# Kernel tuning notes

Hardware: AMD Instinct MI355X
Metric: run time of the kernel (lower is better)

Reference implementation:

```python
import jax, jax.numpy as jnp
import numpy as np

B, T, C = 4, 2048, 1024
N_HEAD = 16
HEAD_SIZE = C // N_HEAD


def setup_inputs() -> dict:
    key = jax.random.key(0)
    ks = jax.random.split(key, 9)
    std = 0.02
    return {
        "x": jax.random.normal(ks[0], (B, T, C), dtype=jnp.float32),
        "Wk": jax.random.normal(ks[1], (C, C), dtype=jnp.float32) * std,
        "bk": jnp.zeros((C,), dtype=jnp.float32),
        "Wq": jax.random.normal(ks[2], (C, C), dtype=jnp.float32) * std,
        "bq": jnp.zeros((C,), dtype=jnp.float32),
        "Wv": jax.random.normal(ks[3], (C, C), dtype=jnp.float32) * std,
        "bv": jnp.zeros((C,), dtype=jnp.float32),
        "Wo": jax.random.normal(ks[4], (C, C), dtype=jnp.float32) * std,
        "bo": jnp.zeros((C,), dtype=jnp.float32),
    }


def reference(x, Wk, bk, Wq, bq, Wv, bv, Wo, bo):
    # QKV projections -> (B, T, H, D)
    k = (x @ Wk + bk).reshape(B, T, N_HEAD, HEAD_SIZE)
    q = (x @ Wq + bq).reshape(B, T, N_HEAD, HEAD_SIZE)
    v = (x @ Wv + bv).reshape(B, T, N_HEAD, HEAD_SIZE)
    # Scaled causal attention scores: (B, H, T, T)
    scale = 1.0 / jnp.sqrt(jnp.asarray(HEAD_SIZE, dtype=x.dtype))
    scores = jnp.einsum("bqhd,bkhd->bhqk", q, k) * scale
    causal = jnp.tril(jnp.ones((T, T), dtype=bool))
    scores = jnp.where(causal, scores, jnp.asarray(-1e10, dtype=x.dtype))
    probs = jax.nn.softmax(scores, axis=-1)
    # Weighted values -> (B, T, H, D) -> (B, T, C)
    y = jnp.einsum("bhqk,bkhd->bqhd", probs, v).reshape(B, T, C)
    # Output projection (dropout rates are 0 / deterministic)
    return y @ Wo + bo
```

## Files before the change

kernel.cpp:

```cpp
#include <hip/hip_runtime.h>
#include <hip/hip_bf16.h>

typedef unsigned short ushort_t;
typedef __attribute__((ext_vector_type(8))) short short8;
typedef __attribute__((ext_vector_type(4))) float floatx4;

#define BATCH 4
#define SEQ   2048
#define CH    1024
#define NHEAD 16
#define HSZ   64
#define MROWS (BATCH * SEQ)

#define GLD16(gptr, lptr) \
    __builtin_amdgcn_global_load_lds((const __attribute__((address_space(1))) unsigned int*)(gptr), \
                                     (__attribute__((address_space(3))) unsigned int*)(lptr), 16, 0, 0)

__device__ inline ushort_t f2b(float f) {
    __hip_bfloat16 h = __float2bfloat16(f);
    return *(ushort_t*)&h;
}
__device__ inline float b2f(ushort_t u) {
    return __bfloat162float(*(__hip_bfloat16*)&u);
}

__global__ void detect_dtype(const ushort_t* __restrict__ x, int* __restrict__ flag) {
    if (threadIdx.x == 0 && blockIdx.x == 0) {
        int cnt = 0;
        for (int i = 0; i < 512; i++) {
            const int e = (x[2 * i] >> 7) & 0xFF;
            if (e >= 100 && e <= 140) cnt++;
        }
        *flag = (cnt >= 400) ? 1 : 0;
    }
}

__global__ __launch_bounds__(256) void convert_wt4(const void* w0, const void* w1,
                                                   const void* w2, const void* w3,
                                                   ushort_t* o0, ushort_t* o1,
                                                   ushort_t* o2, ushort_t* o3,
                                                   const int* __restrict__ flag) {
    __shared__ ushort_t tile[32][33];
    const void* in = (blockIdx.z == 0) ? w0 : (blockIdx.z == 1) ? w1 : (blockIdx.z == 2) ? w2 : w3;
    ushort_t*  out = (blockIdx.z == 0) ? o0 : (blockIdx.z == 1) ? o1 : (blockIdx.z == 2) ? o2 : o3;
    const int am = *flag;
    const int bx = blockIdx.x * 32, by = blockIdx.y * 32;
    const int tx = threadIdx.x & 31, ty = threadIdx.x >> 5;
    #pragma unroll
    for (int r = ty; r < 32; r += 8) {
        const size_t idx = (size_t)(by + r) * CH + bx + tx;
        tile[r][tx] = am ? ((const ushort_t*)in)[idx] : f2b(((const float*)in)[idx]);
    }
    __syncthreads();
    #pragma unroll
    for (int r = ty; r < 32; r += 8)
        out[(size_t)(bx + r) * CH + by + tx] = tile[tx][r];
}

__global__ void convert_bias4(const void* b0, const void* b1, const void* b2, const void* b3,
                              ushort_t* __restrict__ out, const int* __restrict__ flag) {
    const int i = blockIdx.x * 256 + threadIdx.x;
    const int m = i >> 10, idx = i & 1023;
    const void* in = (m == 0) ? b0 : (m == 1) ? b1 : (m == 2) ? b2 : b3;
    out[i] = (*flag) ? ((const ushort_t*)in)[idx] : f2b(((const float*)in)[idx]);
}

__global__ __launch_bounds__(256) void convert_x(const void* __restrict__ in,
                                                 ushort_t* __restrict__ out,
                                                 const int* __restrict__ flag) {
    const int i = (blockIdx.x * 256 + threadIdx.x) * 8;
    if (*flag) {
        *(float4*)&out[i] = *(const float4*)&((const ushort_t*)in)[i];
    } else {
        const float* p = (const float*)in + i;
        float4 f0 = *(const float4*)p;
        float4 f1 = *(const float4*)(p + 4);
        ushort_t t[8] = {f2b(f0.x), f2b(f0.y), f2b(f0.z), f2b(f0.w),
                         f2b(f1.x), f2b(f1.y), f2b(f1.z), f2b(f1.w)};
        *(float4*)&out[i] = *(const float4*)t;
    }
}

__global__ __launch_bounds__(256) void gemm_qkv(const ushort_t* __restrict__ A,
                                                const ushort_t* __restrict__ Bt,
                                                const ushort_t* __restrict__ bias,
                                                ushort_t* __restrict__ Qb,
                                                ushort_t* __restrict__ Kb,
                                                ushort_t* __restrict__ Vt,
                                                float qscale) {
    __shared__ __align__(16) ushort_t As[128 * 32];
    __shared__ __align__(16) ushort_t Bs[128 * 32];
    const int K = CH;
    const int tid = threadIdx.x;
    const int lane = tid & 63, wave = tid >> 6;
    const int lane15 = lane & 15, quad = lane >> 4;
    const int wr = (wave >> 1) * 64, wc = (wave & 1) * 64;
    const int row0 = blockIdx.x * 128, col0 = blockIdx.y * 128;
    const int seg = blockIdx.y >> 3;

    floatx4 acc[4][4];
    #pragma unroll
    for (int i = 0; i < 4; i++)
        #pragma unroll
        for (int j = 0; j < 4; j++) acc[i][j] = {0.f, 0.f, 0.f, 0.f};

    for (int k0 = 0; k0 < K; k0 += 32) {
        #pragma unroll
        for (int l = wave; l < 8; l += 4) {
            GLD16(A  + (size_t)(row0 + l * 16 + (lane >> 2)) * K + k0 + (lane & 3) * 8, &As[l * 512]);
            GLD16(Bt + (size_t)(col0 + l * 16 + (lane >> 2)) * K + k0 + (lane & 3) * 8, &Bs[l * 512]);
        }
        __syncthreads();
        short8 af[4], bfr[4];
        #pragma unroll
        for (int i = 0; i < 4; i++)
            af[i] = *(const short8*)&As[(wr + i * 16 + lane15) * 32 + quad * 8];
        #pragma unroll
        for (int j = 0; j < 4; j++)
            bfr[j] = *(const short8*)&Bs[(wc + j * 16 + lane15) * 32 + quad * 8];
        #pragma unroll
        for (int i = 0; i < 4; i++)
            #pragma unroll
            for (int j = 0; j < 4; j++)
                acc[i][j] = __builtin_amdgcn_mfma_f32_16x16x32_bf16(af[i], bfr[j], acc[i][j], 0, 0, 0);
        __syncthreads();
    }

    #pragma unroll
    for (int j = 0; j < 4; j++) {
        const int col = col0 + wc + j * 16 + lane15;
        const float bv = b2f(bias[col]);
        #pragma unroll
        for (int i = 0; i < 4; i++) {
            const int rowb = row0 + wr + i * 16 + quad * 4;
            if (seg == 0) {
                #pragma unroll
                for (int r = 0; r < 4; r++)
                    Qb[(size_t)(rowb + r) * CH + col] = f2b((acc[i][j][r] + bv) * qscale);
            } else if (seg == 1) {
                const int c = col - 1024;
                #pragma unroll
                for (int r = 0; r < 4; r++)
                    Kb[(size_t)(rowb + r) * CH + c] = f2b(acc[i][j][r] + bv);
            } else {
                const int c = col - 2048;
                ushort_t pk[4];
                #pragma unroll
                for (int r = 0; r < 4; r++) pk[r] = f2b(acc[i][j][r] + bv);
                const int bb = rowb >> 11, t = rowb & 2047;
                *(uint2*)&Vt[((size_t)bb * 1024 + c) * 2048 + t] = *(const uint2*)pk;
            }
        }
    }
}

__global__ __launch_bounds__(256) void gemm_bt(const ushort_t* __restrict__ A,
                                               const ushort_t* __restrict__ Bt,
                                               const ushort_t* __restrict__ bias,
                                               void* __restrict__ Out,
                                               int M, int N, int K,
                                               const int* __restrict__ oflag) {
    __shared__ __align__(16) ushort_t As[128 * 32];
    __shared__ __align__(16) ushort_t Bs[128 * 32];
    const int om = *oflag;
    const int tid = threadIdx.x;
    const int lane = tid & 63, wave = tid >> 6;
    const int lane15 = lane & 15, quad = lane >> 4;
    const int wr = (wave >> 1) * 64, wc = (wave & 1) * 64;
    const int row0 = blockIdx.x * 128, col0 = blockIdx.y * 128;

    floatx4 acc[4][4];
    #pragma unroll
    for (int i = 0; i < 4; i++)
        #pragma unroll
        for (int j = 0; j < 4; j++) acc[i][j] = {0.f, 0.f, 0.f, 0.f};

    for (int k0 = 0; k0 < K; k0 += 32) {
        #pragma unroll
        for (int l = wave; l < 8; l += 4) {
            GLD16(A  + (size_t)(row0 + l * 16 + (lane >> 2)) * K + k0 + (lane & 3) * 8, &As[l * 512]);
            GLD16(Bt + (size_t)(col0 + l * 16 + (lane >> 2)) * K + k0 + (lane & 3) * 8, &Bs[l * 512]);
        }
        __syncthreads();
        short8 af[4], bfr[4];
        #pragma unroll
        for (int i = 0; i < 4; i++)
            af[i] = *(const short8*)&As[(wr + i * 16 + lane15) * 32 + quad * 8];
        #pragma unroll
        for (int j = 0; j < 4; j++)
            bfr[j] = *(const short8*)&Bs[(wc + j * 16 + lane15) * 32 + quad * 8];
        #pragma unroll
        for (int i = 0; i < 4; i++)
            #pragma unroll
            for (int j = 0; j < 4; j++)
                acc[i][j] = __builtin_amdgcn_mfma_f32_16x16x32_bf16(af[i], bfr[j], acc[i][j], 0, 0, 0);
        __syncthreads();
    }

    #pragma unroll
    for (int j = 0; j < 4; j++) {
        const int col = col0 + wc + j * 16 + lane15;
        const float bv = b2f(bias[col]);
        #pragma unroll
        for (int i = 0; i < 4; i++) {
            const int rowb = row0 + wr + i * 16 + quad * 4;
            #pragma unroll
            for (int r = 0; r < 4; r++) {
                const float val = acc[i][j][r] + bv;
                const size_t idx = (size_t)(rowb + r) * N + col;
                if (om) ((ushort_t*)Out)[idx] = f2b(val);
                else    ((float*)Out)[idx] = val;
            }
        }
    }
}

__global__ __launch_bounds__(256) void attn_fwd(ushort_t* __restrict__ QY,
                                                const ushort_t* __restrict__ K,
                                                const ushort_t* __restrict__ Vt) {
    __shared__ __align__(16) ushort_t Ks[2][64 * 64];
    __shared__ __align__(16) ushort_t Vs[2][64 * 64];
    __shared__ __align__(16) ushort_t Ps[4 * 32 * 72];
    const int tid = threadIdx.x;
    const int lane = tid & 63, wave = tid >> 6;
    const int lane15 = lane & 15, quad = lane >> 4;
    const int sw = lane15 & 7;
    const int bid = blockIdx.x;
    const int hb = bid & 63, qslot = bid >> 6;
    const int qb = 15 - qslot;
    const int h = hb & 15, b = hb >> 4;
    const int q0 = qb * 128;
    const size_t baseR = (size_t)b * SEQ * CH + h * HSZ;
    const size_t baseV = ((size_t)b * 1024 + h * HSZ) * SEQ;
    const int rg = lane >> 3, cg = (lane & 7) ^ rg;

    short8 qf[2][2];
    #pragma unroll
    for (int mm = 0; mm < 2; mm++) {
        const ushort_t* qp = QY + baseR + (size_t)(q0 + wave * 32 + mm * 16 + lane15) * CH + quad * 8;
        qf[mm][0] = *(const short8*)qp;
        qf[mm][1] = *(const short8*)(qp + 32);
    }
    const short8 kOnes = (short8)(short)0x3F80;

    floatx4 o[2][5];
    #pragma unroll
    for (int mm = 0; mm < 2; mm++)
        #pragma unroll
        for (int j = 0; j < 5; j++) o[mm][j] = {0.f, 0.f, 0.f, 0.f};

    const int nkt = 2 * qb + 2;
    #pragma unroll
    for (int l = wave; l < 8; l += 4) {
        GLD16(K  + baseR + (size_t)(l * 8 + rg) * CH + cg * 8, &Ks[0][l * 512]);
        GLD16(Vt + baseV + (size_t)(l * 8 + rg) * SEQ + cg * 8, &Vs[0][l * 512]);
    }

    for (int kt = 0; kt < nkt; kt++) {
        __syncthreads();
        const int cur = kt & 1;
        if (kt + 1 < nkt) {
            const int kv1 = (kt + 1) * 64, nb = cur ^ 1;
            #pragma unroll
            for (int l = wave; l < 8; l += 4) {
                GLD16(K  + baseR + (size_t)(kv1 + l * 8 + rg) * CH + cg * 8, &Ks[nb][l * 512]);
                GLD16(Vt + baseV + (size_t)(l * 8 + rg) * SEQ + kv1 + cg * 8, &Vs[nb][l * 512]);
            }
        }
        const int kv0 = kt * 64;
        const int masked = (kt >= 2 * qb);
        #pragma unroll
        for (int mm = 0; mm < 2; mm++) {
            floatx4 s4[4];
            #pragma unroll
            for (int j = 0; j < 4; j++) {
                short8 b0 = *(const short8*)&Ks[cur][(j * 16 + lane15) * 64 + ((quad ^ sw) * 8)];
                short8 b1 = *(const short8*)&Ks[cur][(j * 16 + lane15) * 64 + (((quad + 4) ^ sw) * 8)];
                floatx4 z = {0.f, 0.f, 0.f, 0.f};
                z = __builtin_amdgcn_mfma_f32_16x16x32_bf16(qf[mm][0], b0, z, 0, 0, 0);
                z = __builtin_amdgcn_mfma_f32_16x16x32_bf16(qf[mm][1], b1, z, 0, 0, 0);
                s4[j] = z;
            }
            const int qrow_base = q0 + wave * 32 + mm * 16 + quad * 4;
            if (masked) {
                #pragma unroll
                for (int j = 0; j < 4; j++) {
                    const int col = kv0 + j * 16 + lane15;
                    #pragma unroll
                    for (int r = 0; r < 4; r++)
                        s4[j][r] = (col <= qrow_base + r) ? s4[j][r] : -1e30f;
                }
            }
            #pragma unroll
            for (int j = 0; j < 4; j++)
                #pragma unroll
                for (int r = 0; r < 4; r++)
                    Ps[wave * 2304 + (mm * 16 + quad * 4 + r) * 72 + j * 16 + lane15] =
                        f2b(exp2f(s4[j][r]));
        }

        #pragma unroll
        for (int kk = 0; kk < 2; kk++) {
            #pragma unroll
            for (int mm = 0; mm < 2; mm++) {
                short8 a = *(const short8*)&Ps[wave * 2304 + (mm * 16 + lane15) * 72 + kk * 32 + quad * 8];
                #pragma unroll
                for (int jn = 0; jn < 4; jn++) {
                    short8 bb = *(const short8*)&Vs[cur][(jn * 16 + lane15) * 64 + (((kk * 4 + quad) ^ sw) * 8)];
                    o[mm][jn] = __builtin_amdgcn_mfma_f32_16x16x32_bf16(a, bb, o[mm][jn], 0, 0, 0);
                }
                o[mm][4] = __builtin_amdgcn_mfma_f32_16x16x32_bf16(a, kOnes, o[mm][4], 0, 0, 0);
            }
        }
    }

    #pragma unroll
    for (int mm = 0; mm < 2; mm++)
        #pragma unroll
        for (int r = 0; r < 4; r++) {
            const int qrow = q0 + wave * 32 + mm * 16 + quad * 4 + r;
            const float rinv = 1.0f / fmaxf(o[mm][4][r], 1e-30f);
            #pragma unroll
            for (int jn = 0; jn < 4; jn++)
                QY[baseR + (size_t)qrow * CH + jn * 16 + lane15] = f2b(o[mm][jn][r] * rinv);
        }
}

extern "C" void kernel_launch(void* const* d_in, const int* in_sizes, int n_in,
                              void* d_out, int out_size, void* d_ws, size_t ws_size,
                              hipStream_t stream) {
    const void* x  = d_in[0];
    const void* Wk = d_in[1];
    const void* bk = d_in[2];
    const void* Wq = d_in[3];
    const void* bq = d_in[4];
    const void* Wv = d_in[5];
    const void* bv = d_in[6];
    const void* Wo = d_in[7];
    const void* bo = d_in[8];

    ushort_t* ws    = (ushort_t*)d_ws;
    int*      flag  = (int*)d_ws;
    ushort_t* biasC = ws + 2048;
    ushort_t* WqkvT = ws + 32768;
    ushort_t* WoT   = WqkvT + 3u * (1u << 20);
    ushort_t* xb    = ws + 4227072;
    ushort_t* Qb    = ws + 12615680;
    ushort_t* Kb    = (ushort_t*)d_out;
    ushort_t* VtB   = Kb + (size_t)MROWS * CH;

    detect_dtype<<<1, 64, 0, stream>>>((const ushort_t*)x, flag);

    dim3 tgrid(32, 32, 4);
    convert_wt4<<<tgrid, 256, 0, stream>>>(Wq, Wk, Wv, Wo,
                                           WqkvT, WqkvT + (1u << 20), WqkvT + 2u * (1u << 20), WoT, flag);
    convert_bias4<<<16, 256, 0, stream>>>(bq, bk, bv, bo, biasC, flag);
    convert_x<<<MROWS * CH / (256 * 8), 256, 0, stream>>>(x, xb, flag);

    dim3 qgrid(MROWS / 128, 3 * CH / 128);
    gemm_qkv<<<qgrid, 256, 0, stream>>>(xb, WqkvT, biasC, Qb, Kb, VtB, 0.1803368801f);

    attn_fwd<<<dim3(1024), 256, 0, stream>>>(Qb, Kb, VtB);

    dim3 ogrid(MROWS / 128, CH / 128);
    gemm_bt<<<ogrid, 256, 0, stream>>>(Qb, WoT, biasC + 3072, d_out, MROWS, CH, CH, flag);
}
```

Measured before the change: 287.7 us.

## Keep attention probabilities in registers via transposed MFMA and lane shuffles

The attention kernel now computes S^T (K as the A operand, Q as B) so each lane holds probabilities for one query row. It packs them to bf16 and redistributes them across lanes with shuffles to form the B operand of the PV MFMA, which removes the LDS round trip through the Ps buffer. Output stores become vectorized 8-byte writes. The change also sets launch_bounds occupancy to 4 and parallelizes dtype detection with ballot. The cost is extra shuffle and select instructions in the inner loop, plus more register pressure under the occupancy hint.

```diff
diff --git a/kernel.cpp b/kernel.cpp
--- a/kernel.cpp
+++ b/kernel.cpp
@@ -25,14 +25,14 @@
 }
 
 __global__ void detect_dtype(const ushort_t* __restrict__ x, int* __restrict__ flag) {
-    if (threadIdx.x == 0 && blockIdx.x == 0) {
-        int cnt = 0;
-        for (int i = 0; i < 512; i++) {
-            const int e = (x[2 * i] >> 7) & 0xFF;
-            if (e >= 100 && e <= 140) cnt++;
-        }
-        *flag = (cnt >= 400) ? 1 : 0;
-    }
+    int cnt = 0;
+    #pragma unroll
+    for (int i = 0; i < 8; i++) {
+        const int e = (x[2 * (threadIdx.x * 8 + i)] >> 7) & 0xFF;
+        const unsigned long long m = __ballot(e >= 100 && e <= 140);
+        cnt += (int)__popcll(m);
+    }
+    if (threadIdx.x == 0) *flag = (cnt >= 400) ? 1 : 0;
 }
 
 __global__ __launch_bounds__(256) void convert_wt4(const void* w0, const void* w1,
@@ -215,12 +215,11 @@
     }
 }
 
-__global__ __launch_bounds__(256) void attn_fwd(ushort_t* __restrict__ QY,
-                                                const ushort_t* __restrict__ K,
-                                                const ushort_t* __restrict__ Vt) {
+__global__ __launch_bounds__(256, 4) void attn_fwd(ushort_t* __restrict__ QY,
+                                                   const ushort_t* __restrict__ K,
+                                                   const ushort_t* __restrict__ Vt) {
     __shared__ __align__(16) ushort_t Ks[2][64 * 64];
     __shared__ __align__(16) ushort_t Vs[2][64 * 64];
-    __shared__ __align__(16) ushort_t Ps[4 * 32 * 72];
     const int tid = threadIdx.x;
     const int lane = tid & 63, wave = tid >> 6;
     const int lane15 = lane & 15, quad = lane >> 4;
@@ -233,6 +232,9 @@
     const size_t baseR = (size_t)b * SEQ * CH + h * HSZ;
     const size_t baseV = ((size_t)b * 1024 + h * HSZ) * SEQ;
     const int rg = lane >> 3, cg = (lane & 7) ^ rg;
+    const int srcA = (quad & 1) * 32 + lane15;
+    const int srcB = srcA + 16;
+    const int hi = quad >> 1;
 
     short8 qf[2][2];
     #pragma unroll
@@ -271,59 +273,73 @@
         const int masked = (kt >= 2 * qb);
         #pragma unroll
         for (int mm = 0; mm < 2; mm++) {
-            floatx4 s4[4];
-            #pragma unroll
-            for (int j = 0; j < 4; j++) {
-                short8 b0 = *(const short8*)&Ks[cur][(j * 16 + lane15) * 64 + ((quad ^ sw) * 8)];
-                short8 b1 = *(const short8*)&Ks[cur][(j * 16 + lane15) * 64 + (((quad + 4) ^ sw) * 8)];
+            const int qg = q0 + wave * 32 + mm * 16 + lane15;
+            unsigned int pk[4][2];
+            #pragma unroll
+            for (int i = 0; i < 4; i++) {
+                short8 a0 = *(const short8*)&Ks[cur][(i * 16 + lane15) * 64 + ((quad ^ sw) * 8)];
+                short8 a1 = *(const short8*)&Ks[cur][(i * 16 + lane15) * 64 + (((quad + 4) ^ sw) * 8)];
                 floatx4 z = {0.f, 0.f, 0.f, 0.f};
-                z = __builtin_amdgcn_mfma_f32_16x16x32_bf16(qf[mm][0], b0, z, 0, 0, 0);
-                z = __builtin_amdgcn_mfma_f32_16x16x32_bf16(qf[mm][1], b1, z, 0, 0, 0);
-                s4[j] = z;
-            }
-            const int qrow_base = q0 + wave * 32 + mm * 16 + quad * 4;
-            if (masked) {
-                #pragma unroll
-                for (int j = 0; j < 4; j++) {
-                    const int col = kv0 + j * 16 + lane15;
-                    #pragma unroll
-                    for (int r = 0; r < 4; r++)
-                        s4[j][r] = (col <= qrow_base + r) ? s4[j][r] : -1e30f;
-                }
-            }
-            #pragma unroll
-            for (int j = 0; j < 4; j++)
-                #pragma unroll
-                for (int r = 0; r < 4; r++)
-                    Ps[wave * 2304 + (mm * 16 + quad * 4 + r) * 72 + j * 16 + lane15] =
-                        f2b(exp2f(s4[j][r]));
-        }
-
-        #pragma unroll
-        for (int kk = 0; kk < 2; kk++) {
-            #pragma unroll
-            for (int mm = 0; mm < 2; mm++) {
-                short8 a = *(const short8*)&Ps[wave * 2304 + (mm * 16 + lane15) * 72 + kk * 32 + quad * 8];
+                z = __builtin_amdgcn_mfma_f32_16x16x32_bf16(a0, qf[mm][0], z, 0, 0, 0);
+                z = __builtin_amdgcn_mfma_f32_16x16x32_bf16(a1, qf[mm][1], z, 0, 0, 0);
+                float p[4];
+                #pragma unroll
+                for (int r = 0; r < 4; r++) {
+                    float v = z[r];
+                    if (masked) {
+                        const int kvg = kv0 + i * 16 + quad * 4 + r;
+                        v = (kvg <= qg) ? v : -1e30f;
+                    }
+                    p[r] = exp2f(v);
+                }
+                pk[i][0] = (unsigned int)f2b(p[0]) | ((unsigned int)f2b(p[1]) << 16);
+                pk[i][1] = (unsigned int)f2b(p[2]) | ((unsigned int)f2b(p[3]) << 16);
+            }
+            #pragma unroll
+            for (int kk = 0; kk < 2; kk++) {
+                union { unsigned int u[4]; short8 s8; } pb;
+                {
+                    const unsigned int a0 = __shfl((int)pk[2 * kk + 0][0], srcA, 64);
+                    const unsigned int a1 = __shfl((int)pk[2 * kk + 1][0], srcA, 64);
+                    pb.u[0] = hi ? a1 : a0;
+                }
+                {
+                    const unsigned int a0 = __shfl((int)pk[2 * kk + 0][1], srcA, 64);
+                    const unsigned int a1 = __shfl((int)pk[2 * kk + 1][1], srcA, 64);
+                    pb.u[1] = hi ? a1 : a0;
+                }
+                {
+                    const unsigned int b0 = __shfl((int)pk[2 * kk + 0][0], srcB, 64);
+                    const unsigned int b1 = __shfl((int)pk[2 * kk + 1][0], srcB, 64);
+                    pb.u[2] = hi ? b1 : b0;
+                }
+                {
+                    const unsigned int b0 = __shfl((int)pk[2 * kk + 0][1], srcB, 64);
+                    const unsigned int b1 = __shfl((int)pk[2 * kk + 1][1], srcB, 64);
+                    pb.u[3] = hi ? b1 : b0;
+                }
                 #pragma unroll
                 for (int jn = 0; jn < 4; jn++) {
-                    short8 bb = *(const short8*)&Vs[cur][(jn * 16 + lane15) * 64 + (((kk * 4 + quad) ^ sw) * 8)];
-                    o[mm][jn] = __builtin_amdgcn_mfma_f32_16x16x32_bf16(a, bb, o[mm][jn], 0, 0, 0);
-                }
-                o[mm][4] = __builtin_amdgcn_mfma_f32_16x16x32_bf16(a, kOnes, o[mm][4], 0, 0, 0);
-            }
-        }
-    }
-
-    #pragma unroll
-    for (int mm = 0; mm < 2; mm++)
-        #pragma unroll
-        for (int r = 0; r < 4; r++) {
-            const int qrow = q0 + wave * 32 + mm * 16 + quad * 4 + r;
-            const float rinv = 1.0f / fmaxf(o[mm][4][r], 1e-30f);
-            #pragma unroll
-            for (int jn = 0; jn < 4; jn++)
-                QY[baseR + (size_t)qrow * CH + jn * 16 + lane15] = f2b(o[mm][jn][r] * rinv);
-        }
+                    short8 vf = *(const short8*)&Vs[cur][(jn * 16 + lane15) * 64 + (((kk * 4 + quad) ^ sw) * 8)];
+                    o[mm][jn] = __builtin_amdgcn_mfma_f32_16x16x32_bf16(vf, pb.s8, o[mm][jn], 0, 0, 0);
+                }
+                o[mm][4] = __builtin_amdgcn_mfma_f32_16x16x32_bf16(kOnes, pb.s8, o[mm][4], 0, 0, 0);
+            }
+        }
+    }
+
+    #pragma unroll
+    for (int mm = 0; mm < 2; mm++) {
+        const int qg = q0 + wave * 32 + mm * 16 + lane15;
+        const float rinv = 1.0f / fmaxf(o[mm][4][0], 1e-30f);
+        #pragma unroll
+        for (int jn = 0; jn < 4; jn++) {
+            ushort_t pkk[4];
+            #pragma unroll
+            for (int r = 0; r < 4; r++) pkk[r] = f2b(o[mm][jn][r] * rinv);
+            *(uint2*)&QY[baseR + (size_t)qg * CH + jn * 16 + quad * 4] = *(const uint2*)pkk;
+        }
+    }
 }
 
 extern "C" void kernel_launch(void* const* d_in, const int* in_sizes, int n_in,
```

New measurement: 431.4 us. 49.9% more time.
